# Kernel tuning notes

Measured on AMD Instinct MI355X. Metric: run time of the kernel, lower is better.

Reference implementation:

```python
import jax, jax.numpy as jnp
import numpy as np

B, L, IN_DIM, OUT_DIM = 4, 512, 32, 1
D_MODEL, N_LAYERS = 768, 4
E = 2 * D_MODEL      # d_inner
N = 16               # d_state
K = 4                # d_conv
R = D_MODEL // 16    # dt_rank


def setup_inputs() -> dict:
    key = jax.random.key(0)
    ks = jax.random.split(key, 16)
    p = lambda k, shape, s=0.02: (s * jax.random.normal(k, shape)).astype(jnp.float32)
    inp = {
        'x': jax.random.normal(ks[0], (B, L, IN_DIM), dtype=jnp.float32),
        'in_w': p(ks[1], (D_MODEL, IN_DIM)),
        'in_b': jnp.zeros((D_MODEL,), jnp.float32),
        'in_proj_w': p(ks[2], (N_LAYERS, 2 * E, D_MODEL)),
        'conv_w': p(ks[3], (N_LAYERS, E, K), 0.1),
        'conv_b': jnp.zeros((N_LAYERS, E), jnp.float32),
        'xproj_w': p(ks[4], (N_LAYERS, R + 2 * N, E)),
        'dtproj_w': p(ks[5], (N_LAYERS, E, R), 0.1),
        'dtproj_b': p(ks[6], (N_LAYERS, E), 0.5),
        'A_log': jnp.log(jnp.broadcast_to(jnp.arange(1, N + 1, dtype=jnp.float32), (N_LAYERS, E, N))),
        'D_ssm': jnp.ones((N_LAYERS, E), jnp.float32),
        'outproj_w': p(ks[7], (N_LAYERS, D_MODEL, E)),
        'norm_w': jnp.ones((N_LAYERS, D_MODEL), jnp.float32),
        'normf_w': jnp.ones((D_MODEL,), jnp.float32),
        'out_w': p(ks[8], (OUT_DIM, D_MODEL)),
        'out_b': jnp.zeros((OUT_DIM,), jnp.float32),
    }
    return inp


def _rmsnorm(x, w, eps=1e-5):
    return x * jax.lax.rsqrt(jnp.mean(x * x, axis=-1, keepdims=True) + eps) * w


def _selective_scan(u, delta, A, Bm, C, D):
    # u, delta: [B,L,E]; A: [E,N]; Bm, C: [B,L,N]; D: [E]
    dA = jnp.exp(delta[..., None] * A)                       # [B,L,E,N]
    dBu = delta[..., None] * Bm[:, :, None, :] * u[..., None]  # [B,L,E,N]

    def step(h, inp):
        dA_t, dBu_t, C_t = inp
        h = dA_t * h + dBu_t                                  # [B,E,N]
        y = jnp.einsum('ben,bn->be', h, C_t)
        return h, y

    h0 = jnp.zeros((u.shape[0], u.shape[2], A.shape[1]), u.dtype)
    _, ys = jax.lax.scan(step, h0, (dA.transpose(1, 0, 2, 3), dBu.transpose(1, 0, 2, 3), C.transpose(1, 0, 2)))
    return ys.transpose(1, 0, 2) + u * D                      # [B,L,E]


def _mamba_block(xn, in_proj_w, conv_w, conv_b, xproj_w, dtproj_w, dtproj_b, A_log, D_ssm, outproj_w):
    xz = xn @ in_proj_w.T                                     # [B,L,2E]
    xc, res = xz[..., :E], xz[..., E:]
    # depthwise causal conv1d
    xt = xc.transpose(0, 2, 1)                                # [B,E,L]
    y = jax.lax.conv_general_dilated(xt, conv_w[:, None, :], (1,), [(K - 1, 0)],
                                     feature_group_count=E,
                                     dimension_numbers=('NCH', 'OIH', 'NCH'))
    u = jax.nn.silu((y + conv_b[None, :, None]).transpose(0, 2, 1))  # [B,L,E]
    x_dbl = u @ xproj_w.T                                     # [B,L,R+2N]
    dt, Bm, C = x_dbl[..., :R], x_dbl[..., R:R + N], x_dbl[..., R + N:]
    delta = jax.nn.softplus(dt @ dtproj_w.T + dtproj_b)       # [B,L,E]
    A = -jnp.exp(A_log)                                       # [E,N]
    y = _selective_scan(u, delta, A, Bm, C, D_ssm)
    y = y * jax.nn.silu(res)
    return y @ outproj_w.T                                    # [B,L,D_MODEL]


def reference(x, in_w, in_b, in_proj_w, conv_w, conv_b, xproj_w, dtproj_w, dtproj_b,
              A_log, D_ssm, outproj_w, norm_w, normf_w, out_w, out_b):
    h = x @ in_w.T + in_b                                     # [B,L,D_MODEL]
    for i in range(N_LAYERS):
        h = h + _mamba_block(_rmsnorm(h, norm_w[i]), in_proj_w[i], conv_w[i], conv_b[i],
                             xproj_w[i], dtproj_w[i], dtproj_b[i], A_log[i], D_ssm[i], outproj_w[i])
    h = _rmsnorm(h, normf_w)
    last = h[:, -1, :]
    out = jax.nn.sigmoid(last @ out_w.T + out_b)              # [B,OUT_DIM]
    return out.reshape(-1)
```

## Files before the change

kernel.cpp:

```cpp
#include <hip/hip_runtime.h>
#include <hip/hip_bf16.h>
#include <cmath>

#define BATCH 4
#define SEQ 512
#define TOK (BATCH*SEQ)
#define DMODEL 768
#define EDIM 1536
#define TWOE 3072
#define RDIM 48
#define NSTATE 16
#define RN2 80
#define CONVK 4
#define XSPLIT 6
#define CH 8
#define CL (SEQ/CH)
#define EBLK 64

#define EPI_STORE 0
#define EPI_BIAS 1
#define EPI_BIAS_SOFTPLUS 2
#define EPI_ADD 3

typedef short bf16x8 __attribute__((ext_vector_type(8)));
typedef float f32x4 __attribute__((ext_vector_type(4)));

__device__ __forceinline__ unsigned short f2bf(float f) {
  unsigned int u = __builtin_bit_cast(unsigned int, f);
  u = (u + 0x7FFFu + ((u >> 16) & 1u)) >> 16;
  return (unsigned short)u;
}

template<int BM, int BN, int EPI, bool NB>
__global__ __launch_bounds__(256) void gemm_mfma(
    const unsigned short* __restrict__ Abf,
    const unsigned short* __restrict__ Wbf,
    float* __restrict__ C, int ldc, int Kk, int ldk,
    int Nvalid, size_t zCstride, const float* __restrict__ bias) {
  constexpr int WM = BM / 2, WN = BN / 2;
  constexpr int IT = WM / 16, JT = WN / 16;
  __shared__ __align__(16) char smem[(BM + BN) * 128];
  char* ldsA = smem;
  char* ldsB = smem + BM * 128;

  const int tid = threadIdx.x;
  const int wid = tid >> 6, lane = tid & 63;
  const int m0 = blockIdx.y * BM, n0 = blockIdx.x * BN;
  const int wm = (wid >> 1) * WM, wn = (wid & 1) * WN;
  const int quad = lane >> 4, l15 = lane & 15;

  const int srow = lane >> 3;
  const int kc = (lane & 7) ^ srow;
  const int koff = blockIdx.z * Kk;
  C += (size_t)blockIdx.z * zCstride;
  const unsigned short* gA = Abf + (size_t)(m0 + srow) * ldk + kc * 8 + koff;
  const unsigned short* gB = Wbf + (size_t)(n0 + srow) * ldk + kc * 8 + koff;

  f32x4 acc[IT][JT] = {};

  for (int k0 = 0; k0 < Kk; k0 += 64) {
#pragma unroll
    for (int c = wid; c < BM / 8; c += 4)
      __builtin_amdgcn_global_load_lds(
          (const __attribute__((address_space(1))) void*)(gA + (size_t)(c * 8) * ldk + k0),
          (__attribute__((address_space(3))) void*)(ldsA + c * 1024), 16, 0, 0);
#pragma unroll
    for (int c = wid; c < BN / 8; c += 4)
      __builtin_amdgcn_global_load_lds(
          (const __attribute__((address_space(1))) void*)(gB + (size_t)(c * 8) * ldk + k0),
          (__attribute__((address_space(3))) void*)(ldsB + c * 1024), 16, 0, 0);
    asm volatile("s_waitcnt vmcnt(0)" ::: "memory");
    __syncthreads();
#pragma unroll
    for (int t = 0; t < 2; ++t) {
      const int cc = t * 4 + quad;
      bf16x8 av[IT], bv[JT];
#pragma unroll
      for (int i = 0; i < IT; ++i) {
        const int row = wm + i * 16 + l15;
        const int slot = cc ^ (row & 7);
        av[i] = *(const bf16x8*)(ldsA + row * 128 + slot * 16);
      }
#pragma unroll
      for (int j = 0; j < JT; ++j) {
        const int row = wn + j * 16 + l15;
        const int slot = cc ^ (row & 7);
        bv[j] = *(const bf16x8*)(ldsB + row * 128 + slot * 16);
      }
#pragma unroll
      for (int i = 0; i < IT; ++i)
#pragma unroll
        for (int j = 0; j < JT; ++j)
          acc[i][j] = __builtin_amdgcn_mfma_f32_16x16x32_bf16(av[i], bv[j], acc[i][j], 0, 0, 0);
    }
    __syncthreads();
  }

#pragma unroll
  for (int i = 0; i < IT; ++i) {
#pragma unroll
    for (int r = 0; r < 4; ++r) {
      const int m = m0 + wm + i * 16 + quad * 4 + r;
      float* crow = C + (size_t)m * ldc + n0 + wn;
#pragma unroll
      for (int j = 0; j < JT; ++j) {
        const int n = j * 16 + l15;
        if (NB && (n0 + wn + n) >= Nvalid) continue;
        float v = acc[i][j][r];
        if (EPI == EPI_BIAS_SOFTPLUS) {
          v += bias[n0 + wn + n];
          v = (v > 20.f) ? v : log1pf(expf(v));
        }
        if (EPI == EPI_ADD) v += crow[n];
        crow[n] = v;
      }
    }
  }
}

__global__ __launch_bounds__(256) void reduce_part_k(
    const float* __restrict__ part, float* __restrict__ out,
    unsigned short* __restrict__ dtbf) {
  int i = (blockIdx.x * 256 + threadIdx.x) * 4;
  if (i >= TOK * RN2) return;
  float4 s = *(const float4*)(part + i);
#pragma unroll
  for (int z = 1; z < XSPLIT; ++z) {
    float4 v = *(const float4*)(part + (size_t)z * TOK * RN2 + i);
    s.x += v.x; s.y += v.y; s.z += v.z; s.w += v.w;
  }
  *(float4*)(out + i) = s;
  int row = i / RN2, col = i % RN2;
  if (col < RDIM) {
    ushort4 r;
    r.x = f2bf(s.x); r.y = f2bf(s.y); r.z = f2bf(s.z); r.w = f2bf(s.w);
    *(ushort4*)(dtbf + (size_t)row * 64 + col) = r;
  }
  if (col < 16) {
    ushort4 z0 = {0, 0, 0, 0};
    *(ushort4*)(dtbf + (size_t)row * 64 + RDIM + col) = z0;
  }
}

#define CAST_N1 (4LL*TWOE*DMODEL)
#define CAST_N2 (4LL*DMODEL*EDIM)
#define CAST_N3 (4LL*128*EDIM)
#define CAST_N4 (4LL*EDIM*64)
#define CAST_TOT (CAST_N1+CAST_N2+CAST_N3+CAST_N4)
__global__ __launch_bounds__(256) void cast_all_k(
    const float* __restrict__ inw, const float* __restrict__ outw,
    const float* __restrict__ xw, const float* __restrict__ dtw,
    unsigned short* __restrict__ w_in, unsigned short* __restrict__ w_out,
    unsigned short* __restrict__ w_x, unsigned short* __restrict__ w_dt) {
  long long i = ((long long)blockIdx.x * 256 + threadIdx.x) * 4;
  if (i >= CAST_TOT) return;
  const float* src = nullptr;
  unsigned short* dst;
  if (i < CAST_N1) {
    src = inw + i; dst = w_in + i;
  } else if (i < CAST_N1 + CAST_N2) {
    long long j = i - CAST_N1;
    src = outw + j; dst = w_out + j;
  } else if (i < CAST_N1 + CAST_N2 + CAST_N3) {
    long long j = i - CAST_N1 - CAST_N2;
    int l = (int)(j / (128LL * EDIM));
    int rem = (int)(j % (128LL * EDIM));
    int r = rem / EDIM, c = rem % EDIM;
    dst = w_x + j;
    if (r < RN2) src = xw + ((long long)l * RN2 + r) * EDIM + c;
  } else {
    long long j = i - CAST_N1 - CAST_N2 - CAST_N3;
    int l = (int)(j / (EDIM * 64LL));
    int rem = (int)(j % (EDIM * 64LL));
    int row = rem / 64, col = rem % 64;
    dst = w_dt + j;
    if (col < RDIM) src = dtw + ((long long)l * EDIM + row) * RDIM + col;
  }
  ushort4 r = {0, 0, 0, 0};
  if (src) {
    float4 v = *(const float4*)src;
    r.x = f2bf(v.x); r.y = f2bf(v.y); r.z = f2bf(v.z); r.w = f2bf(v.w);
  }
  *(ushort4*)dst = r;
}

template<int EPI>
__global__ __launch_bounds__(256) void gemm_tn(
    const float* __restrict__ A, int lda,
    const float* __restrict__ W, int ldw,
    const float* __restrict__ bias,
    float* __restrict__ C, int ldc,
    int M, int Nn, int Kk) {
  __shared__ float As[16][68];
  __shared__ float Bs[16][68];
  const int tid = threadIdx.x;
  const int m0 = blockIdx.y * 64, n0 = blockIdx.x * 64;
  const int lr = tid >> 2;
  const int lc = (tid & 3) << 2;
  const int ty = tid >> 4, tx = tid & 15;
  float acc[4][4] = {};

  for (int k0 = 0; k0 < Kk; k0 += 16) {
    {
      int m = m0 + lr;
      float4 v = make_float4(0.f, 0.f, 0.f, 0.f);
      if (m < M) v = *(const float4*)(A + (size_t)m * lda + k0 + lc);
      As[lc + 0][lr] = v.x; As[lc + 1][lr] = v.y;
      As[lc + 2][lr] = v.z; As[lc + 3][lr] = v.w;
    }
    {
      int nn = n0 + lr;
      float4 v = make_float4(0.f, 0.f, 0.f, 0.f);
      if (nn < Nn) v = *(const float4*)(W + (size_t)nn * ldw + k0 + lc);
      Bs[lc + 0][lr] = v.x; Bs[lc + 1][lr] = v.y;
      Bs[lc + 2][lr] = v.z; Bs[lc + 3][lr] = v.w;
    }
    __syncthreads();
#pragma unroll
    for (int kk = 0; kk < 16; ++kk) {
      float av[4], bv[4];
#pragma unroll
      for (int i = 0; i < 4; ++i) av[i] = As[kk][ty * 4 + i];
#pragma unroll
      for (int j = 0; j < 4; ++j) bv[j] = Bs[kk][tx * 4 + j];
#pragma unroll
      for (int i = 0; i < 4; ++i)
#pragma unroll
        for (int j = 0; j < 4; ++j)
          acc[i][j] += av[i] * bv[j];
    }
    __syncthreads();
  }

#pragma unroll
  for (int i = 0; i < 4; ++i) {
    int m = m0 + ty * 4 + i;
    if (m >= M) continue;
#pragma unroll
    for (int j = 0; j < 4; ++j) {
      int nn = n0 + tx * 4 + j;
      if (nn >= Nn) continue;
      float v = acc[i][j];
      float* cp = C + (size_t)m * ldc + nn;
      if (EPI == EPI_BIAS) v += bias[nn];
      if (EPI == EPI_ADD) v += *cp;
      *cp = v;
    }
  }
}

__global__ __launch_bounds__(256) void rmsnorm_k(
    const float* __restrict__ x, const float* __restrict__ w,
    unsigned short* __restrict__ o, int D) {
  const int t = blockIdx.x;
  const float* row = x + (size_t)t * D;
  __shared__ float ls[8];
  const int lane = threadIdx.x & 63, wave = threadIdx.x >> 6;
  float s = 0.f;
  for (int i = threadIdx.x; i < D; i += 256) { float v = row[i]; s += v * v; }
  for (int off = 32; off; off >>= 1) s += __shfl_down(s, off);
  if (lane == 0) ls[wave] = s;
  __syncthreads();
  float tot = ls[0] + ls[1] + ls[2] + ls[3];
  float rs = rsqrtf(tot / (float)D + 1e-5f);
  for (int i = threadIdx.x; i < D; i += 256)
    o[(size_t)t * D + i] = f2bf(row[i] * rs * w[i]);
}

__global__ __launch_bounds__(256) void conv_silu4_k(
    const float* __restrict__ xz, const float* __restrict__ cw,
    const float* __restrict__ cb, float* __restrict__ u,
    unsigned short* __restrict__ ubf) {
  const int idx = blockIdx.x * 256 + threadIdx.x;
  const int ec = (idx % (EDIM / 4)) * 4;
  const int tok = idx / (EDIM / 4);
  const int tl = tok & (SEQ - 1);
  float4 acc = *(const float4*)(cb + ec);
  float wt[16];
  *(float4*)(wt + 0)  = *(const float4*)(cw + ec * 4);
  *(float4*)(wt + 4)  = *(const float4*)(cw + ec * 4 + 4);
  *(float4*)(wt + 8)  = *(const float4*)(cw + ec * 4 + 8);
  *(float4*)(wt + 12) = *(const float4*)(cw + ec * 4 + 12);
#pragma unroll
  for (int j = 0; j < CONVK; ++j) {
    int tt = tl - (CONVK - 1) + j;
    if (tt >= 0) {
      float4 xv = *(const float4*)(xz + (size_t)(tok - (CONVK - 1) + j) * TWOE + ec);
      acc.x += xv.x * wt[0 * 4 + j];
      acc.y += xv.y * wt[1 * 4 + j];
      acc.z += xv.z * wt[2 * 4 + j];
      acc.w += xv.w * wt[3 * 4 + j];
    }
  }
  float4 s;
  s.x = acc.x / (1.f + __expf(-acc.x));
  s.y = acc.y / (1.f + __expf(-acc.y));
  s.z = acc.z / (1.f + __expf(-acc.z));
  s.w = acc.w / (1.f + __expf(-acc.w));
  *(float4*)(u + (size_t)idx * 4) = s;
  ushort4 r;
  r.x = f2bf(s.x); r.y = f2bf(s.y); r.z = f2bf(s.z); r.w = f2bf(s.w);
  *(ushort4*)(ubf + (size_t)idx * 4) = r;
}


__global__ __launch_bounds__(256) void scan_p1(
    const float* __restrict__ delta, const float* __restrict__ u,
    const float* __restrict__ xdbl, const float* __restrict__ A_log,
    float* __restrict__ hend, float* __restrict__ aprod) {
  const int tid = threadIdx.x;
  const int g = tid >> 2, nq = tid & 3;
  const int nch = blockIdx.x & (CH - 1);
  const int rem = blockIdx.x >> 3;
  const int e0 = (rem % (EDIM / EBLK)) * EBLK;
  const int b = rem / (EDIM / EBLK);
  const int e = e0 + g;
  float4 Al = *(const float4*)(A_log + (size_t)e * NSTATE + nq * 4);
  float4 A4;
  A4.x = -__expf(Al.x); A4.y = -__expf(Al.y);
  A4.z = -__expf(Al.z); A4.w = -__expf(Al.w);
  const size_t base = (size_t)b * SEQ + nch * CL;

  __shared__ float s_dv[2][8][EBLK];
  __shared__ float s_uv[2][8][EBLK];
  __shared__ float s_B[2][8][16];

  const float* gp0 = nullptr; float* ld0 = nullptr; size_t st0 = 0; int off0 = 0;
  const float* gp1 = nullptr; float* ld1 = nullptr; size_t st1 = 0; int off1 = 0;
  if (tid < 128) {
    int j = tid >> 4, q = tid & 15;
    gp0 = delta + (base + j) * EDIM + e0 + q * 4; st0 = 8 * (size_t)EDIM;
    ld0 = &s_dv[0][j][q * 4]; off0 = 8 * EBLK;
    if (tid < 32) {
      int jj = tid >> 2, nn = (tid & 3) * 4;
      gp1 = xdbl + (base + jj) * RN2 + RDIM + nn; st1 = 8 * (size_t)RN2;
      ld1 = &s_B[0][jj][nn]; off1 = 8 * 16;
    }
  } else {
    int r = tid - 128;
    int j = r >> 4, q = r & 15;
    gp0 = u + (base + j) * EDIM + e0 + q * 4; st0 = 8 * (size_t)EDIM;
    ld0 = &s_uv[0][j][q * 4]; off0 = 8 * EBLK;
  }
  if (ld0) { float4 v = *(const float4*)gp0; gp0 += st0; *(float4*)ld0 = v; }
  if (ld1) { float4 v = *(const float4*)gp1; gp1 += st1; *(float4*)ld1 = v; }

  float4 h = {0.f, 0.f, 0.f, 0.f};
  float sdv = 0.f;
  for (int it = 0; it < CL / 8; ++it) {
    const int cur = it & 1;
    const bool hn = (it < CL / 8 - 1);
    float4 nv0, nv1;
    if (hn && ld0) { nv0 = *(const float4*)gp0; gp0 += st0; }
    if (hn && ld1) { nv1 = *(const float4*)gp1; gp1 += st1; }
    __syncthreads();
#pragma unroll
    for (int j = 0; j < 8; ++j) {
      float dv = s_dv[cur][j][g];
      float uv = s_uv[cur][j][g];
      float4 Bv = *(const float4*)&s_B[cur][j][nq * 4];
      float duv = dv * uv;
      h.x = __expf(dv * A4.x) * h.x + duv * Bv.x;
      h.y = __expf(dv * A4.y) * h.y + duv * Bv.y;
      h.z = __expf(dv * A4.z) * h.z + duv * Bv.z;
      h.w = __expf(dv * A4.w) * h.w + duv * Bv.w;
      sdv += dv;
    }
    if (hn && ld0) *(float4*)(ld0 + (cur ^ 1) * off0) = nv0;
    if (hn && ld1) *(float4*)(ld1 + (cur ^ 1) * off1) = nv1;
  }
  size_t o = (((size_t)b * CH + nch) * EDIM + e) * NSTATE + nq * 4;
  *(float4*)(hend + o) = h;
  float4 ap;
  ap.x = __expf(A4.x * sdv); ap.y = __expf(A4.y * sdv);
  ap.z = __expf(A4.z * sdv); ap.w = __expf(A4.w * sdv);
  *(float4*)(aprod + o) = ap;
}

__global__ __launch_bounds__(256) void scan_p2(
    const float* __restrict__ delta, const float* __restrict__ u,
    const float* __restrict__ xdbl, const float* __restrict__ xz,
    const float* __restrict__ A_log, const float* __restrict__ D_ssm,
    const float* __restrict__ hend, const float* __restrict__ aprod,
    unsigned short* __restrict__ y) {
  const int tid = threadIdx.x;
  const int g = tid >> 2, nq = tid & 3;
  const int nch = blockIdx.x & (CH - 1);
  const int rem = blockIdx.x >> 3;
  const int e0 = (rem % (EDIM / EBLK)) * EBLK;
  const int b = rem / (EDIM / EBLK);
  const int e = e0 + g;
  float4 Al = *(const float4*)(A_log + (size_t)e * NSTATE + nq * 4);
  float4 A4;
  A4.x = -__expf(Al.x); A4.y = -__expf(Al.y);
  A4.z = -__expf(Al.z); A4.w = -__expf(Al.w);
  const float Dv = D_ssm[e];
  const size_t base = (size_t)b * SEQ + nch * CL;

  __shared__ float s_dv[2][8][EBLK];
  __shared__ float s_uv[2][8][EBLK];
  __shared__ float s_rs[2][8][EBLK];
  __shared__ float s_B[2][8][16];
  __shared__ float s_C[2][8][16];

  const float* gp0 = nullptr; float* ld0 = nullptr; size_t st0 = 0; int off0 = 0;
  const float* gp1 = nullptr; float* ld1 = nullptr; size_t st1 = 0; int off1 = 0;
  if (tid < 128) {
    int j = tid >> 4, q = tid & 15;
    gp0 = delta + (base + j) * EDIM + e0 + q * 4; st0 = 8 * (size_t)EDIM;
    ld0 = &s_dv[0][j][q * 4]; off0 = 8 * EBLK;
    gp1 = xz + (base + j) * TWOE + EDIM + e0 + q * 4; st1 = 8 * (size_t)TWOE;
    ld1 = &s_rs[0][j][q * 4]; off1 = 8 * EBLK;
  } else {
    int r = tid - 128;
    int j = r >> 4, q = r & 15;
    gp0 = u + (base + j) * EDIM + e0 + q * 4; st0 = 8 * (size_t)EDIM;
    ld0 = &s_uv[0][j][q * 4]; off0 = 8 * EBLK;
    if (r < 32) {
      int jj = r >> 2, nn = (r & 3) * 4;
      gp1 = xdbl + (base + jj) * RN2 + RDIM + nn; st1 = 8 * (size_t)RN2;
      ld1 = &s_B[0][jj][nn]; off1 = 8 * 16;
    } else if (r < 64) {
      int r2 = r - 32;
      int jj = r2 >> 2, nn = (r2 & 3) * 4;
      gp1 = xdbl + (base + jj) * RN2 + RDIM + NSTATE + nn; st1 = 8 * (size_t)RN2;
      ld1 = &s_C[0][jj][nn]; off1 = 8 * 16;
    }
  }
  if (ld0) { float4 v = *(const float4*)gp0; gp0 += st0; *(float4*)ld0 = v; }
  if (ld1) { float4 v = *(const float4*)gp1; gp1 += st1; *(float4*)ld1 = v; }

  float4 h = {0.f, 0.f, 0.f, 0.f};
  for (int c = 0; c < nch; ++c) {
    size_t o = (((size_t)b * CH + c) * EDIM + e) * NSTATE + nq * 4;
    float4 he = *(const float4*)(hend + o);
    float4 ap = *(const float4*)(aprod + o);
    h.x = he.x + ap.x * h.x;
    h.y = he.y + ap.y * h.y;
    h.z = he.z + ap.z * h.z;
    h.w = he.w + ap.w * h.w;
  }

  float pva = 0.f, pvb = 0.f;
  unsigned short* yp = y + base * EDIM + e;
  for (int it = 0; it < CL / 8; ++it) {
    const int cur = it & 1;
    const bool hn = (it < CL / 8 - 1);
    float4 nv0, nv1;
    if (hn && ld0) { nv0 = *(const float4*)gp0; gp0 += st0; }
    if (hn && ld1) { nv1 = *(const float4*)gp1; gp1 += st1; }
    __syncthreads();
#pragma unroll
    for (int j = 0; j < 8; ++j) {
      float dv = s_dv[cur][j][g];
      float uv = s_uv[cur][j][g];
      float4 Bv = *(const float4*)&s_B[cur][j][nq * 4];
      float4 Cv = *(const float4*)&s_C[cur][j][nq * 4];
      float duv = dv * uv;
      h.x = __expf(dv * A4.x) * h.x + duv * Bv.x;
      h.y = __expf(dv * A4.y) * h.y + duv * Bv.y;
      h.z = __expf(dv * A4.z) * h.z + duv * Bv.z;
      h.w = __expf(dv * A4.w) * h.w + duv * Bv.w;
      float p = h.x * Cv.x + h.y * Cv.y + h.z * Cv.z + h.w * Cv.w;
      p += __shfl_xor(p, 1);
      p += __shfl_xor(p, 2);
      pva = (j == nq) ? p : pva;
      pvb = (j == nq + 4) ? p : pvb;
    }
    {
      float uv0 = s_uv[cur][nq][g],     rs0 = s_rs[cur][nq][g];
      float uv1 = s_uv[cur][nq + 4][g], rs1 = s_rs[cur][nq + 4][g];
      float sil0 = rs0 / (1.f + __expf(-rs0));
      float sil1 = rs1 / (1.f + __expf(-rs1));
      yp[(size_t)(it * 8 + nq) * EDIM]     = f2bf((pva + uv0 * Dv) * sil0);
      yp[(size_t)(it * 8 + nq + 4) * EDIM] = f2bf((pvb + uv1 * Dv) * sil1);
    }
    if (hn && ld0) *(float4*)(ld0 + (cur ^ 1) * off0) = nv0;
    if (hn && ld1) *(float4*)(ld1 + (cur ^ 1) * off1) = nv1;
  }
}

__global__ __launch_bounds__(256) void final_k(
    const float* __restrict__ h, const float* __restrict__ nw,
    const float* __restrict__ ow, const float* __restrict__ ob,
    float* __restrict__ out) {
  const int b = blockIdx.x;
  const float* row = h + ((size_t)(b * SEQ + SEQ - 1)) * DMODEL;
  __shared__ float ls[8];
  __shared__ float ls2[8];
  const int lane = threadIdx.x & 63, wave = threadIdx.x >> 6;
  float s = 0.f;
  for (int i = threadIdx.x; i < DMODEL; i += 256) { float v = row[i]; s += v * v; }
  for (int off = 32; off; off >>= 1) s += __shfl_down(s, off);
  if (lane == 0) ls[wave] = s;
  __syncthreads();
  float tot = ls[0] + ls[1] + ls[2] + ls[3];
  float rs = rsqrtf(tot / (float)DMODEL + 1e-5f);
  float d = 0.f;
  for (int i = threadIdx.x; i < DMODEL; i += 256)
    d += row[i] * rs * nw[i] * ow[i];
  for (int off = 32; off; off >>= 1) d += __shfl_down(d, off);
  if (lane == 0) ls2[wave] = d;
  __syncthreads();
  if (threadIdx.x == 0) {
    float dot = ls2[0] + ls2[1] + ls2[2] + ls2[3] + ob[0];
    out[b] = 1.f / (1.f + expf(-dot));
  }
}

extern "C" void kernel_launch(void* const* d_in, const int* in_sizes, int n_in,
                              void* d_out, int out_size, void* d_ws, size_t ws_size,
                              hipStream_t stream) {
  const float* x         = (const float*)d_in[0];
  const float* in_w      = (const float*)d_in[1];
  const float* in_b      = (const float*)d_in[2];
  const float* in_proj_w = (const float*)d_in[3];
  const float* conv_w    = (const float*)d_in[4];
  const float* conv_b    = (const float*)d_in[5];
  const float* xproj_w   = (const float*)d_in[6];
  const float* dtproj_w  = (const float*)d_in[7];
  const float* dtproj_b  = (const float*)d_in[8];
  const float* A_log     = (const float*)d_in[9];
  const float* D_ssm     = (const float*)d_in[10];
  const float* outproj_w = (const float*)d_in[11];
  const float* norm_w    = (const float*)d_in[12];
  const float* normf_w   = (const float*)d_in[13];
  const float* out_w     = (const float*)d_in[14];
  const float* out_b     = (const float*)d_in[15];
  float* out = (float*)d_out;
  float* ws  = (float*)d_ws;

  float* h     = ws;
  float* xz    = h + (size_t)TOK * DMODEL;
  float* u     = xz + (size_t)TOK * TWOE;
  float* xdb   = u + (size_t)TOK * EDIM;
  float* dl    = xdb + (size_t)TOK * RN2;
  float* part  = dl + (size_t)TOK * EDIM;
  float* hend  = part + (size_t)XSPLIT * TOK * RN2;
  float* aprod = hend + (size_t)BATCH * CH * EDIM * NSTATE;
  unsigned short* xn_bf = (unsigned short*)(aprod + (size_t)BATCH * CH * EDIM * NSTATE);
  unsigned short* y_bf  = xn_bf + (size_t)TOK * DMODEL;
  unsigned short* u_bf  = y_bf + (size_t)TOK * EDIM;
  unsigned short* dt_bf = u_bf + (size_t)TOK * EDIM;
  unsigned short* w_in  = dt_bf + (size_t)TOK * 64;
  unsigned short* w_out = w_in + (size_t)4 * TWOE * DMODEL;
  unsigned short* w_x   = w_out + (size_t)4 * DMODEL * EDIM;
  unsigned short* w_dt  = w_x + (size_t)4 * 128 * EDIM;

  dim3 blk(256);

  cast_all_k<<<(int)((CAST_TOT / 4 + 255) / 256), blk, 0, stream>>>(
      in_proj_w, outproj_w, xproj_w, dtproj_w, w_in, w_out, w_x, w_dt);

  gemm_tn<EPI_BIAS><<<dim3(DMODEL / 64, TOK / 64), blk, 0, stream>>>(
      x, 32, in_w, 32, in_b, h, DMODEL, TOK, DMODEL, 32);

  for (int l = 0; l < 4; ++l) {
    rmsnorm_k<<<TOK, 256, 0, stream>>>(h, norm_w + l * DMODEL, xn_bf, DMODEL);

    gemm_mfma<128, 128, EPI_STORE, false><<<dim3(TWOE / 128, TOK / 128, 1), blk, 0, stream>>>(
        xn_bf, w_in + (size_t)l * TWOE * DMODEL, xz, TWOE, DMODEL, DMODEL, TWOE, 0, nullptr);

    conv_silu4_k<<<(TOK * EDIM / 4) / 256, 256, 0, stream>>>(
        xz, conv_w + l * EDIM * CONVK, conv_b + l * EDIM, u, u_bf);

    gemm_mfma<64, 64, EPI_STORE, true><<<dim3(2, TOK / 64, XSPLIT), blk, 0, stream>>>(
        u_bf, w_x + (size_t)l * 128 * EDIM, part, RN2, EDIM / XSPLIT, EDIM, RN2,
        (size_t)TOK * RN2, nullptr);
    reduce_part_k<<<(TOK * RN2 / 4 + 255) / 256, 256, 0, stream>>>(part, xdb, dt_bf);

    gemm_mfma<128, 64, EPI_BIAS_SOFTPLUS, false><<<dim3(EDIM / 64, TOK / 128, 1), blk, 0, stream>>>(
        dt_bf, w_dt + (size_t)l * EDIM * 64, dl, EDIM, 64, 64, EDIM, 0,
        dtproj_b + l * EDIM);

    scan_p1<<<BATCH * (EDIM / EBLK) * CH, 256, 0, stream>>>(
        dl, u, xdb, A_log + (size_t)l * EDIM * NSTATE, hend, aprod);
    scan_p2<<<BATCH * (EDIM / EBLK) * CH, 256, 0, stream>>>(
        dl, u, xdb, xz, A_log + (size_t)l * EDIM * NSTATE, D_ssm + l * EDIM,
        hend, aprod, y_bf);

    gemm_mfma<128, 64, EPI_ADD, false><<<dim3(DMODEL / 64, TOK / 128, 1), blk, 0, stream>>>(
        y_bf, w_out + (size_t)l * DMODEL * EDIM, h, DMODEL, EDIM, EDIM, DMODEL, 0, nullptr);
  }

  final_k<<<BATCH, 256, 0, stream>>>(h, normf_w, out_w, out_b, out);
}
```

Baseline: 656.8 us.

## Drop x_proj split-K reduction, fuse dt cast, retile conv and small GEMMs

The x_proj GEMM no longer splits K six ways with a separate reduction kernel. It runs un-split over 64 blocks and writes both the fp32 x_dbl and the padded bf16 dt operand from its epilogue, removing one launch and the partial-sum traffic. The conv+SiLU kernel now has each thread produce 4 consecutive tokens, reusing 7 loaded rows instead of 16. The dt_proj and out_proj GEMMs switch to 64x64 tiles for more blocks. The risk is that the un-split x_proj GEMM has very low parallelism with a long K loop.

```diff
diff --git a/kernel.cpp b/kernel.cpp
--- a/kernel.cpp
+++ b/kernel.cpp
@@ -12,7 +12,6 @@
 #define NSTATE 16
 #define RN2 80
 #define CONVK 4
-#define XSPLIT 6
 #define CH 8
 #define CL (SEQ/CH)
 #define EBLK 64
@@ -21,6 +20,7 @@
 #define EPI_BIAS 1
 #define EPI_BIAS_SOFTPLUS 2
 #define EPI_ADD 3
+#define EPI_XPROJ 4
 
 typedef short bf16x8 __attribute__((ext_vector_type(8)));
 typedef float f32x4 __attribute__((ext_vector_type(4)));
@@ -36,7 +36,8 @@
     const unsigned short* __restrict__ Abf,
     const unsigned short* __restrict__ Wbf,
     float* __restrict__ C, int ldc, int Kk, int ldk,
-    int Nvalid, size_t zCstride, const float* __restrict__ bias) {
+    int Nvalid, size_t zCstride, const float* __restrict__ bias,
+    unsigned short* __restrict__ dtbf) {
   constexpr int WM = BM / 2, WN = BN / 2;
   constexpr int IT = WM / 16, JT = WN / 16;
   __shared__ __align__(16) char smem[(BM + BN) * 128];
@@ -105,40 +106,23 @@
 #pragma unroll
       for (int j = 0; j < JT; ++j) {
         const int n = j * 16 + l15;
-        if (NB && (n0 + wn + n) >= Nvalid) continue;
+        const int ng = n0 + wn + n;
         float v = acc[i][j][r];
-        if (EPI == EPI_BIAS_SOFTPLUS) {
-          v += bias[n0 + wn + n];
-          v = (v > 20.f) ? v : log1pf(expf(v));
+        if (EPI == EPI_XPROJ) {
+          if (ng < Nvalid) crow[n] = v;
+          if (ng < 64)
+            dtbf[(size_t)m * 64 + ng] = (ng < RDIM) ? f2bf(v) : (unsigned short)0;
+        } else {
+          if (NB && ng >= Nvalid) continue;
+          if (EPI == EPI_BIAS_SOFTPLUS) {
+            v += bias[ng];
+            v = (v > 20.f) ? v : log1pf(expf(v));
+          }
+          if (EPI == EPI_ADD) v += crow[n];
+          crow[n] = v;
         }
-        if (EPI == EPI_ADD) v += crow[n];
-        crow[n] = v;
       }
     }
-  }
-}
-
-__global__ __launch_bounds__(256) void reduce_part_k(
-    const float* __restrict__ part, float* __restrict__ out,
-    unsigned short* __restrict__ dtbf) {
-  int i = (blockIdx.x * 256 + threadIdx.x) * 4;
-  if (i >= TOK * RN2) return;
-  float4 s = *(const float4*)(part + i);
-#pragma unroll
-  for (int z = 1; z < XSPLIT; ++z) {
-    float4 v = *(const float4*)(part + (size_t)z * TOK * RN2 + i);
-    s.x += v.x; s.y += v.y; s.z += v.z; s.w += v.w;
-  }
-  *(float4*)(out + i) = s;
-  int row = i / RN2, col = i % RN2;
-  if (col < RDIM) {
-    ushort4 r;
-    r.x = f2bf(s.x); r.y = f2bf(s.y); r.z = f2bf(s.z); r.w = f2bf(s.w);
-    *(ushort4*)(dtbf + (size_t)row * 64 + col) = r;
-  }
-  if (col < 16) {
-    ushort4 z0 = {0, 0, 0, 0};
-    *(ushort4*)(dtbf + (size_t)row * 64 + RDIM + col) = z0;
   }
 }
 
@@ -267,42 +251,50 @@
     o[(size_t)t * D + i] = f2bf(row[i] * rs * w[i]);
 }
 
-__global__ __launch_bounds__(256) void conv_silu4_k(
+__global__ __launch_bounds__(256) void conv_silu16_k(
     const float* __restrict__ xz, const float* __restrict__ cw,
     const float* __restrict__ cb, float* __restrict__ u,
     unsigned short* __restrict__ ubf) {
   const int idx = blockIdx.x * 256 + threadIdx.x;
   const int ec = (idx % (EDIM / 4)) * 4;
-  const int tok = idx / (EDIM / 4);
-  const int tl = tok & (SEQ - 1);
-  float4 acc = *(const float4*)(cb + ec);
+  const int tg = idx / (EDIM / 4);
+  const int t0 = tg * 4;
+  const int tl0 = t0 & (SEQ - 1);
+  float4 bias4 = *(const float4*)(cb + ec);
   float wt[16];
   *(float4*)(wt + 0)  = *(const float4*)(cw + ec * 4);
   *(float4*)(wt + 4)  = *(const float4*)(cw + ec * 4 + 4);
   *(float4*)(wt + 8)  = *(const float4*)(cw + ec * 4 + 8);
   *(float4*)(wt + 12) = *(const float4*)(cw + ec * 4 + 12);
-#pragma unroll
-  for (int j = 0; j < CONVK; ++j) {
-    int tt = tl - (CONVK - 1) + j;
-    if (tt >= 0) {
-      float4 xv = *(const float4*)(xz + (size_t)(tok - (CONVK - 1) + j) * TWOE + ec);
-      acc.x += xv.x * wt[0 * 4 + j];
-      acc.y += xv.y * wt[1 * 4 + j];
-      acc.z += xv.z * wt[2 * 4 + j];
-      acc.w += xv.w * wt[3 * 4 + j];
-    }
-  }
-  float4 s;
-  s.x = acc.x / (1.f + __expf(-acc.x));
-  s.y = acc.y / (1.f + __expf(-acc.y));
-  s.z = acc.z / (1.f + __expf(-acc.z));
-  s.w = acc.w / (1.f + __expf(-acc.w));
-  *(float4*)(u + (size_t)idx * 4) = s;
-  ushort4 r;
-  r.x = f2bf(s.x); r.y = f2bf(s.y); r.z = f2bf(s.z); r.w = f2bf(s.w);
-  *(ushort4*)(ubf + (size_t)idx * 4) = r;
-}
-
+  float4 xv[7];
+#pragma unroll
+  for (int i = 0; i < 7; ++i) {
+    int rel = i - 3;
+    if (rel < 0 && tl0 == 0) { xv[i] = make_float4(0.f, 0.f, 0.f, 0.f); }
+    else xv[i] = *(const float4*)(xz + (size_t)(t0 + rel) * TWOE + ec);
+  }
+#pragma unroll
+  for (int k = 0; k < 4; ++k) {
+    float4 acc = bias4;
+#pragma unroll
+    for (int q = 0; q < CONVK; ++q) {
+      float4 xvv = xv[k + q];
+      acc.x += xvv.x * wt[0 * 4 + q];
+      acc.y += xvv.y * wt[1 * 4 + q];
+      acc.z += xvv.z * wt[2 * 4 + q];
+      acc.w += xvv.w * wt[3 * 4 + q];
+    }
+    float4 s;
+    s.x = acc.x / (1.f + __expf(-acc.x));
+    s.y = acc.y / (1.f + __expf(-acc.y));
+    s.z = acc.z / (1.f + __expf(-acc.z));
+    s.w = acc.w / (1.f + __expf(-acc.w));
+    *(float4*)(u + (size_t)(t0 + k) * EDIM + ec) = s;
+    ushort4 r;
+    r.x = f2bf(s.x); r.y = f2bf(s.y); r.z = f2bf(s.z); r.w = f2bf(s.w);
+    *(ushort4*)(ubf + (size_t)(t0 + k) * EDIM + ec) = r;
+  }
+}
 
 __global__ __launch_bounds__(256) void scan_p1(
     const float* __restrict__ delta, const float* __restrict__ u,
@@ -535,8 +527,7 @@
   float* u     = xz + (size_t)TOK * TWOE;
   float* xdb   = u + (size_t)TOK * EDIM;
   float* dl    = xdb + (size_t)TOK * RN2;
-  float* part  = dl + (size_t)TOK * EDIM;
-  float* hend  = part + (size_t)XSPLIT * TOK * RN2;
+  float* hend  = dl + (size_t)TOK * EDIM;
   float* aprod = hend + (size_t)BATCH * CH * EDIM * NSTATE;
   unsigned short* xn_bf = (unsigned short*)(aprod + (size_t)BATCH * CH * EDIM * NSTATE);
   unsigned short* y_bf  = xn_bf + (size_t)TOK * DMODEL;
@@ -559,19 +550,19 @@
     rmsnorm_k<<<TOK, 256, 0, stream>>>(h, norm_w + l * DMODEL, xn_bf, DMODEL);
 
     gemm_mfma<128, 128, EPI_STORE, false><<<dim3(TWOE / 128, TOK / 128, 1), blk, 0, stream>>>(
-        xn_bf, w_in + (size_t)l * TWOE * DMODEL, xz, TWOE, DMODEL, DMODEL, TWOE, 0, nullptr);
-
-    conv_silu4_k<<<(TOK * EDIM / 4) / 256, 256, 0, stream>>>(
+        xn_bf, w_in + (size_t)l * TWOE * DMODEL, xz, TWOE, DMODEL, DMODEL, TWOE, 0,
+        nullptr, nullptr);
+
+    conv_silu16_k<<<(TOK / 4) * (EDIM / 4) / 256, 256, 0, stream>>>(
         xz, conv_w + l * EDIM * CONVK, conv_b + l * EDIM, u, u_bf);
 
-    gemm_mfma<64, 64, EPI_STORE, true><<<dim3(2, TOK / 64, XSPLIT), blk, 0, stream>>>(
-        u_bf, w_x + (size_t)l * 128 * EDIM, part, RN2, EDIM / XSPLIT, EDIM, RN2,
-        (size_t)TOK * RN2, nullptr);
-    reduce_part_k<<<(TOK * RN2 / 4 + 255) / 256, 256, 0, stream>>>(part, xdb, dt_bf);
-
-    gemm_mfma<128, 64, EPI_BIAS_SOFTPLUS, false><<<dim3(EDIM / 64, TOK / 128, 1), blk, 0, stream>>>(
+    gemm_mfma<64, 64, EPI_XPROJ, true><<<dim3(2, TOK / 64, 1), blk, 0, stream>>>(
+        u_bf, w_x + (size_t)l * 128 * EDIM, xdb, RN2, EDIM, EDIM, RN2, 0,
+        nullptr, dt_bf);
+
+    gemm_mfma<64, 64, EPI_BIAS_SOFTPLUS, false><<<dim3(EDIM / 64, TOK / 64, 1), blk, 0, stream>>>(
         dt_bf, w_dt + (size_t)l * EDIM * 64, dl, EDIM, 64, 64, EDIM, 0,
-        dtproj_b + l * EDIM);
+        dtproj_b + l * EDIM, nullptr);
 
     scan_p1<<<BATCH * (EDIM / EBLK) * CH, 256, 0, stream>>>(
         dl, u, xdb, A_log + (size_t)l * EDIM * NSTATE, hend, aprod);
@@ -579,8 +570,9 @@
         dl, u, xdb, xz, A_log + (size_t)l * EDIM * NSTATE, D_ssm + l * EDIM,
         hend, aprod, y_bf);
 
-    gemm_mfma<128, 64, EPI_ADD, false><<<dim3(DMODEL / 64, TOK / 128, 1), blk, 0, stream>>>(
-        y_bf, w_out + (size_t)l * DMODEL * EDIM, h, DMODEL, EDIM, EDIM, DMODEL, 0, nullptr);
+    gemm_mfma<64, 64, EPI_ADD, false><<<dim3(DMODEL / 64, TOK / 64, 1), blk, 0, stream>>>(
+        y_bf, w_out + (size_t)l * DMODEL * EDIM, h, DMODEL, EDIM, EDIM, DMODEL, 0,
+        nullptr, nullptr);
   }
 
   final_k<<<BATCH, 256, 0, stream>>>(h, normf_w, out_w, out_b, out);
```

Result: faster. 612.7 us (-6.7%).
